# Kernel tuning notes

Measured on AMD Instinct MI355X. Metric: run time of the kernel, lower is better.

The kernel has to match this reference:

```python
import jax, jax.numpy as jnp
import numpy as np

VOCAB, ED, HW, HS, NC = 100000, 200, 100, 100, 10
B, S, W = 128, 40, 50


def setup_inputs() -> dict:
    key = jax.random.key(0)
    ks = jax.random.split(key, 24)
    def p(k, shape, s=0.05):
        return jax.random.normal(k, shape, dtype=jnp.float32) * s
    emb = p(ks[0], (VOCAB, ED)).at[VOCAB - 1].set(0.0)  # padding_idx = vocab-1
    d = dict(
        x=jax.random.randint(ks[23], (B, S, W), 0, VOCAB),
        emb=emb,
        # word bidirectional GRU (forward + backward cells), torch gate order r,z,n
        w_Wih_f=p(ks[1], (3 * HW, ED)), w_bih_f=p(ks[2], (3 * HW,)), w_bhh_f=p(ks[3], (3 * HW,)),
        w_Wih_b=p(ks[4], (3 * HW, ED)), w_bih_b=p(ks[5], (3 * HW,)), w_bhh_b=p(ks[6], (3 * HW,)),
        # word attention
        wa_W=p(ks[7], (2 * HW, 2 * HW)), wa_b=p(ks[8], (2 * HW,)), wa_ctx=p(ks[9], (2 * HW,)),
        # sentence bidirectional GRU (input = 2*HW)
        s_Wih_f=p(ks[10], (3 * HS, 2 * HW)), s_bih_f=p(ks[11], (3 * HS,)), s_bhh_f=p(ks[12], (3 * HS,)),
        s_Wih_b=p(ks[13], (3 * HS, 2 * HW)), s_bih_b=p(ks[14], (3 * HS,)), s_bhh_b=p(ks[15], (3 * HS,)),
        # sentence attention
        sa_W=p(ks[16], (2 * HS, 2 * HS)), sa_b=p(ks[17], (2 * HS,)), sa_ctx=p(ks[18], (2 * HS,)),
        # classifier
        fc_W=p(ks[19], (NC, 2 * HS)), fc_b=p(ks[20], (NC,)),
    )
    return d


def _gru0(x, Wih, bih, bhh, H):
    # GRU cell from zero hidden state: W_hh @ h0 == 0, only b_hh survives.
    g = x @ Wih.T + bih  # [..., 3H], gate order r, z, n
    r = jax.nn.sigmoid(g[..., :H] + bhh[:H])
    z = jax.nn.sigmoid(g[..., H:2 * H] + bhh[H:2 * H])
    n = jnp.tanh(g[..., 2 * H:] + r * bhh[2 * H:])
    return (1.0 - z) * n  # h' = (1-z)*n + z*0


def _bigru0(x, Wf, bf, bhf, Wb, bb, bhb, H):
    # one-timestep bidirectional GRU: fwd and bwd cells both see zero state
    return jnp.concatenate([_gru0(x, Wf, bf, bhf, H), _gru0(x, Wb, bb, bhb, H)], axis=-1)


def _attn(x, Wa, ba, ctx):
    # additive attention pooling over the second-to-last axis
    scores = jnp.einsum('...nd,d->...n', jnp.tanh(x @ Wa.T + ba), ctx)
    alpha = jax.nn.softmax(scores, axis=-1)
    return jnp.einsum('...n,...nd->...d', alpha, x)


def reference(x, emb, w_Wih_f, w_bih_f, w_bhh_f, w_Wih_b, w_bih_b, w_bhh_b,
              wa_W, wa_b, wa_ctx, s_Wih_f, s_bih_f, s_bhh_f, s_Wih_b, s_bih_b, s_bhh_b,
              sa_W, sa_b, sa_ctx, fc_W, fc_b):
    e = emb[x]                                                   # [B,S,W,ED]
    wenc = _bigru0(e, w_Wih_f, w_bih_f, w_bhh_f, w_Wih_b, w_bih_b, w_bhh_b, HW)  # [B,S,W,2HW]
    svec = _attn(wenc, wa_W, wa_b, wa_ctx)                       # [B,S,2HW]
    senc = _bigru0(svec, s_Wih_f, s_bih_f, s_bhh_f, s_Wih_b, s_bih_b, s_bhh_b, HS)  # [B,S,2HS]
    dvec = _attn(senc, sa_W, sa_b, sa_ctx)                       # [B,2HS]
    logits = dvec @ fc_W.T + fc_b                                # [B,NC]
    return jax.nn.log_softmax(logits, axis=1)
```

## Files before the change

### kernel.cpp

```cpp
#include <hip/hip_runtime.h>
#include <math.h>

#define NB    128
#define NS    40
#define NW    50
#define ED    200
#define NHW   100
#define FEAT  200
#define NC    10
#define VOCABM1 99999
#define KL2E  1.4426950408889634f

#define BB       20736ull
#define OFF_PGW  0ull
#define OFF_PAW  (14ull*BB)
#define OFF_PGS  (OFF_PAW + 5ull*BB)
#define OFF_PAS  (OFF_PGS + 14ull*BB)
#define OFF_SV   846336ull
#define OFF_DV   2894336ull
#define WS_NEED  4194304ull

#define SLOT   20736
#define HST    400
#define HBYTES 20000

typedef short bf16x8 __attribute__((ext_vector_type(8)));
typedef float f32x4  __attribute__((ext_vector_type(4)));
typedef unsigned u32x4 __attribute__((ext_vector_type(4)));

__device__ __forceinline__ unsigned short f2bf(float f) {
    unsigned int u = __float_as_uint(f);
    u += 0x7fffu + ((u >> 16) & 1u);
    return (unsigned short)(u >> 16);
}
__device__ __forceinline__ float bf2f(short s) {
    return __uint_as_float(((unsigned int)(unsigned short)s) << 16);
}
__device__ __forceinline__ float frcp(float x) { return __builtin_amdgcn_rcpf(x); }
#if __has_builtin(__builtin_amdgcn_exp2f)
__device__ __forceinline__ float fexp2(float x){ return __builtin_amdgcn_exp2f(x); }
#else
__device__ __forceinline__ float fexp2(float x){ return exp2f(x); }
#endif
__device__ __forceinline__ float fsig(float x) { return frcp(1.f + __expf(-x)); }
__device__ __forceinline__ float ftanh(float x){ return 1.f - 2.f*frcp(1.f + __expf(2.f*x)); }

__device__ __forceinline__ unsigned cvtpk(float lo, float hi) {
    unsigned r;
    asm("v_cvt_pk_bf16_f32 %0, %1, %2" : "=v"(r) : "v"(lo), "v"(hi));
    return r;
}

__device__ __forceinline__ void gld16(const void* g, void* l) {
    __builtin_amdgcn_global_load_lds(
        (const __attribute__((address_space(1))) void*)g,
        (__attribute__((address_space(3))) void*)l, 16, 0, 0);
}

__device__ __forceinline__ void stageBlob(char* __restrict__ dst,
                                          const char* __restrict__ src, int tid)
{
    #pragma unroll
    for (int u = 0; u < 5; ++u)
        gld16(src + (size_t)(u * 256 + tid) * 16, dst + (size_t)(u * 256 + tid) * 16);
    if (tid < 16)
        gld16(src + (size_t)(1280 + tid) * 16, dst + (size_t)(1280 + tid) * 16);
}

__device__ __forceinline__ bf16x8 pack8(float4 a, float4 b) {
    u32x4 t;
    t[0] = cvtpk(a.x, a.y); t[1] = cvtpk(a.z, a.w);
    t[2] = cvtpk(b.x, b.y); t[3] = cvtpk(b.z, b.w);
    return __builtin_bit_cast(bf16x8, t);
}

__global__ void pack_kernel(
    const float* __restrict__ wWf, const float* __restrict__ wbif, const float* __restrict__ wbhf,
    const float* __restrict__ wWb, const float* __restrict__ wbib, const float* __restrict__ wbhb,
    const float* __restrict__ waW, const float* __restrict__ wab, const float* __restrict__ wactx,
    const float* __restrict__ sWf, const float* __restrict__ sbif, const float* __restrict__ sbhf,
    const float* __restrict__ sWb, const float* __restrict__ sbib, const float* __restrict__ sbhb,
    const float* __restrict__ saW, const float* __restrict__ sab, const float* __restrict__ sactx,
    char* __restrict__ ws)
{
    const int b = blockIdx.x, tid = threadIdx.x;
    const bool word = b < 19;
    const int lb = word ? b : b - 19;
    char* blob;
    if (lb < 14) blob = ws + (word ? OFF_PGW : OFF_PGS) + (size_t)lb * BB;
    else         blob = ws + (word ? OFF_PAW : OFF_PAS) + (size_t)(lb - 14) * BB;

    for (int i = tid; i < (int)(BB / 4); i += 256) ((unsigned*)blob)[i] = 0u;
    __syncthreads();

    unsigned short* w16 = (unsigned short*)blob;
    if (lb < 14) {
        const int dir = lb / 7, c = lb % 7;
        const float* W   = word ? (dir ? wWb : wWf) : (dir ? sWb : sWf);
        const float* bih = word ? (dir ? wbib : wbif) : (dir ? sbib : sbif);
        const float* bhh = word ? (dir ? wbhb : wbhf) : (dir ? sbhb : sbhf);
        for (int e = tid; e < 48 * 200; e += 256) {
            const int row = e / 200, k = e - row * 200;
            const int gate = row >> 4, j = c * 16 + (row & 15);
            if (j < NHW) w16[row * 216 + k] = f2bf(W[(size_t)(gate * NHW + j) * ED + k]);
        }
        if (tid < 64) {
            const int sect = tid >> 4, j = c * 16 + (tid & 15);
            float v = 0.f;
            if (j < NHW) {
                if (sect == 0)      v = -KL2E * (bih[j] + bhh[j]);
                else if (sect == 1) v =  KL2E * (bih[NHW + j] + bhh[NHW + j]);
                else if (sect == 2) v = 2.f * KL2E * bih[2 * NHW + j];
                else                v = 2.f * KL2E * bhh[2 * NHW + j];
            }
            ((float*)(blob + (size_t)(tid >> 2) * 432 + 400))[tid & 3] = v;
        }
    } else {
        const int cb = lb - 14;
        const float* W  = word ? waW : saW;
        const float* ab = word ? wab : sab;
        const float* cx = word ? wactx : sactx;
        for (int e = tid; e < 48 * 200; e += 256) {
            const int row = e / 200, k = e - row * 200;
            const int d = cb * 48 + row;
            if (d < FEAT) w16[row * 216 + k] = f2bf(W[(size_t)d * FEAT + k]);
        }
        if (tid < 48) {
            const int d = cb * 48 + tid;
            float ab2 = 0.f, cxn = 0.f;
            if (d < FEAT) { ab2 = 2.f * KL2E * ab[d]; cxn = -2.f * cx[d]; }
            ((float*)(blob + (size_t)(tid >> 2) * 432 + 400))[tid & 3] = ab2;
            ((float*)(blob + (size_t)(12 + (tid >> 2)) * 432 + 400))[tid & 3] = cxn;
        }
    }
}

template<bool WORD>
__global__ __launch_bounds__(256, 4) void han_kernel(
    const int* __restrict__ xtok,
    const void* __restrict__ Ain,
    const char* __restrict__ gpk,
    const char* __restrict__ apk,
    const int nvalid,
    unsigned short* __restrict__ Out)
{
    __shared__ __align__(16) char smem[2 * SLOT + 2 * HBYTES];
    char* bufs = smem;
    char* Hsh  = smem + 2 * SLOT;

    const int tid  = threadIdx.x;
    const int lane = tid & 63, wv = tid >> 6;
    const int sent = wv >> 1, half = wv & 1;
    const int ln15 = lane & 15, q = lane >> 4;
    const long g   = (long)blockIdx.x * 2 + sent;
    char* Hme = Hsh + (size_t)sent * HBYTES;
    float* sc_sh = (float*)Hme;
    float* al_sh = (float*)(Hme + 256);
    float* part  = (float*)(Hme + 512);

    stageBlob(bufs, gpk, tid);

    bf16x8 af[2][7];
    if (WORD) {
        const float* emb = (const float*)Ain;
        #pragma unroll
        for (int Mt = 0; Mt < 2; ++Mt) {
            const int item = half * 32 + Mt * 16 + ln15;
            int tok = VOCABM1;
            if (item < nvalid) tok = xtok[g * nvalid + item];
            const float4* rp = (const float4*)(emb + (long)tok * ED);
            #pragma unroll
            for (int kc = 0; kc < 6; ++kc)
                af[Mt][kc] = pack8(rp[kc * 8 + q * 2], rp[kc * 8 + q * 2 + 1]);
            af[Mt][6] = (q == 0) ? pack8(rp[48], rp[49]) : (bf16x8)(short)0;
        }
    } else {
        const char* sv = (const char*)Ain;
        #pragma unroll
        for (int Mt = 0; Mt < 2; ++Mt) {
            const int item = half * 32 + Mt * 16 + ln15;
            const int ic = item < nvalid ? item : nvalid - 1;
            const char* rp = sv + (g * nvalid + ic) * 400;
            #pragma unroll
            for (int kc = 0; kc < 7; ++kc) {
                bf16x8 v = (bf16x8)(short)0;
                if (item < nvalid && (kc < 6 || q == 0))
                    v = *(const bf16x8*)(rp + kc * 64 + q * 16);
                af[Mt][kc] = v;
            }
        }
    }

    __syncthreads();

    bf16x8 hf[2][7];
    float sacc[2][4] = {{0.f}};

    for (int s = 0; s < 19; ++s) {
        {
            const int t = (s + 1 <= 18) ? (s + 1) : 18;
            const char* nb = (t < 14) ? gpk + (size_t)t * BB
                                      : apk + (size_t)(t - 14) * BB;
            stageBlob(bufs + (size_t)((s + 1) & 1) * SLOT, nb, tid);
        }
        char* cur = bufs + (size_t)(s & 1) * SLOT;

        if (s < 14) {
            f32x4 a0[2] = {}, a1[2] = {}, a2[2] = {};
            #pragma unroll
            for (int kc = 0; kc < 7; ++kc) {
                bf16x8 b0 = (bf16x8)(short)0, b1 = (bf16x8)(short)0, b2 = (bf16x8)(short)0;
                if (kc < 6 || q == 0) {
                    b0 = *(const bf16x8*)(cur + (size_t)(0  + ln15) * 432 + kc * 64 + q * 16);
                    b1 = *(const bf16x8*)(cur + (size_t)(16 + ln15) * 432 + kc * 64 + q * 16);
                    b2 = *(const bf16x8*)(cur + (size_t)(32 + ln15) * 432 + kc * 64 + q * 16);
                }
                #pragma unroll
                for (int Mt = 0; Mt < 2; ++Mt) {
                    a0[Mt] = __builtin_amdgcn_mfma_f32_16x16x32_bf16(b0, af[Mt][kc], a0[Mt], 0, 0, 0);
                    a1[Mt] = __builtin_amdgcn_mfma_f32_16x16x32_bf16(b1, af[Mt][kc], a1[Mt], 0, 0, 0);
                    a2[Mt] = __builtin_amdgcn_mfma_f32_16x16x32_bf16(b2, af[Mt][kc], a2[Mt], 0, 0, 0);
                }
            }
            const int dir = s / 7, cc = s - dir * 7;
            if (cc * 16 + q * 4 < NHW) {
                const f32x4 bR = *(const f32x4*)(cur + (size_t)(0  + q) * 432 + 400);
                const f32x4 bZ = *(const f32x4*)(cur + (size_t)(4  + q) * 432 + 400);
                const f32x4 bN = *(const f32x4*)(cur + (size_t)(8  + q) * 432 + 400);
                const f32x4 hN = *(const f32x4*)(cur + (size_t)(12 + q) * 432 + 400);
                const int ub = dir * NHW + cc * 16 + q * 4;
                #pragma unroll
                for (int Mt = 0; Mt < 2; ++Mt) {
                    const int item = half * 32 + Mt * 16 + ln15;
                    float h[4];
                    #pragma unroll
                    for (int rg = 0; rg < 4; ++rg) {
                        const float r  = frcp(1.f + fexp2(fmaf(a0[Mt][rg], -KL2E, bR[rg])));
                        const float zc = frcp(1.f + fexp2(fmaf(a1[Mt][rg],  KL2E, bZ[rg])));
                        const float t  = frcp(1.f + fexp2(fmaf(a2[Mt][rg], 2.f * KL2E,
                                                  fmaf(r, hN[rg], bN[rg]))));
                        h[rg] = zc * (1.f - 2.f * t);
                    }
                    if (item < nvalid) {
                        uint2 o; o.x = cvtpk(h[0], h[1]); o.y = cvtpk(h[2], h[3]);
                        *(uint2*)(Hme + (size_t)item * HST + ub * 2) = o;
                    }
                }
            }
        } else {
            if (s == 14) {
                #pragma unroll
                for (int Mt = 0; Mt < 2; ++Mt) {
                    const int item = half * 32 + Mt * 16 + ln15;
                    #pragma unroll
                    for (int kc = 0; kc < 7; ++kc) {
                        bf16x8 v = (bf16x8)(short)0;
                        if (item < nvalid && (kc < 6 || q == 0))
                            v = *(const bf16x8*)(Hme + (size_t)item * HST + kc * 64 + q * 16);
                        hf[Mt][kc] = v;
                    }
                }
            }
            f32x4 ac[2][3] = {};
            #pragma unroll
            for (int kc = 0; kc < 7; ++kc) {
                bf16x8 b0 = (bf16x8)(short)0, b1 = (bf16x8)(short)0, b2 = (bf16x8)(short)0;
                if (kc < 6 || q == 0) {
                    b0 = *(const bf16x8*)(cur + (size_t)(0  + ln15) * 432 + kc * 64 + q * 16);
                    b1 = *(const bf16x8*)(cur + (size_t)(16 + ln15) * 432 + kc * 64 + q * 16);
                    b2 = *(const bf16x8*)(cur + (size_t)(32 + ln15) * 432 + kc * 64 + q * 16);
                }
                #pragma unroll
                for (int Mt = 0; Mt < 2; ++Mt) {
                    ac[Mt][0] = __builtin_amdgcn_mfma_f32_16x16x32_bf16(hf[Mt][kc], b0, ac[Mt][0], 0, 0, 0);
                    ac[Mt][1] = __builtin_amdgcn_mfma_f32_16x16x32_bf16(hf[Mt][kc], b1, ac[Mt][1], 0, 0, 0);
                    ac[Mt][2] = __builtin_amdgcn_mfma_f32_16x16x32_bf16(hf[Mt][kc], b2, ac[Mt][2], 0, 0, 0);
                }
            }
            #pragma unroll
            for (int Nt = 0; Nt < 3; ++Nt) {
                const int bo = 4 * (Nt * 16 + ln15);
                const float ab2 = *(const float*)(cur + (size_t)(bo >> 4) * 432 + 400 + (bo & 15));
                const int co = 192 + bo;
                const float cxn = *(const float*)(cur + (size_t)(co >> 4) * 432 + 400 + (co & 15));
                #pragma unroll
                for (int Mt = 0; Mt < 2; ++Mt)
                    #pragma unroll
                    for (int rg = 0; rg < 4; ++rg) {
                        const float u = frcp(1.f + fexp2(fmaf(ac[Mt][Nt][rg], 2.f * KL2E, ab2)));
                        sacc[Mt][rg] = fmaf(u, cxn, sacc[Mt][rg]);
                    }
            }
        }
        __syncthreads();
    }

    #pragma unroll
    for (int Mt = 0; Mt < 2; ++Mt)
        #pragma unroll
        for (int rg = 0; rg < 4; ++rg) {
            float v = sacc[Mt][rg];
            v += __shfl_xor(v, 1); v += __shfl_xor(v, 2);
            v += __shfl_xor(v, 4); v += __shfl_xor(v, 8);
            sacc[Mt][rg] = v;
        }
    if (ln15 == 0) {
        #pragma unroll
        for (int Mt = 0; Mt < 2; ++Mt)
            #pragma unroll
            for (int rg = 0; rg < 4; ++rg)
                sc_sh[half * 32 + Mt * 16 + q * 4 + rg] = sacc[Mt][rg];
    }
    __syncthreads();

    {
        const float sv0 = (lane < nvalid) ? sc_sh[lane] : -1e30f;
        float m = sv0;
        m = fmaxf(m, __shfl_xor(m, 1));  m = fmaxf(m, __shfl_xor(m, 2));
        m = fmaxf(m, __shfl_xor(m, 4));  m = fmaxf(m, __shfl_xor(m, 8));
        m = fmaxf(m, __shfl_xor(m, 16)); m = fmaxf(m, __shfl_xor(m, 32));
        const float e = (lane < nvalid) ? fexp2((sv0 - m) * KL2E) : 0.f;
        float ss = e;
        ss += __shfl_xor(ss, 1);  ss += __shfl_xor(ss, 2);
        ss += __shfl_xor(ss, 4);  ss += __shfl_xor(ss, 8);
        ss += __shfl_xor(ss, 16); ss += __shfl_xor(ss, 32);
        if (half == 0) al_sh[lane] = e * frcp(ss);
    }
    __syncthreads();

    {
        const float aM0 = al_sh[half * 32 + ln15];
        const float aM1 = al_sh[half * 32 + 16 + ln15];
        #pragma unroll
        for (int kc = 0; kc < 7; ++kc) {
            float p[8];
            #pragma unroll
            for (int j = 0; j < 8; ++j)
                p[j] = aM0 * bf2f(hf[0][kc][j]) + aM1 * bf2f(hf[1][kc][j]);
            #pragma unroll
            for (int j = 0; j < 8; ++j) {
                p[j] += __shfl_xor(p[j], 1); p[j] += __shfl_xor(p[j], 2);
                p[j] += __shfl_xor(p[j], 4); p[j] += __shfl_xor(p[j], 8);
            }
            if (ln15 == 0) {
                float* dst = part + (size_t)half * 224 + kc * 32 + q * 8;
                f32x4 v0 = {p[0], p[1], p[2], p[3]};
                f32x4 v1 = {p[4], p[5], p[6], p[7]};
                *(f32x4*)dst = v0; *(f32x4*)(dst + 4) = v1;
            }
        }
    }
    __syncthreads();

    if (tid < 100) {
        const int sl = tid / 50, i = tid - sl * 50;
        const float* pg = (const float*)(Hsh + (size_t)sl * HBYTES + 512);
        const float* pa = pg;
        const float* pb = pg + 224;
        uint2 o;
        o.x = cvtpk(pa[i * 4 + 0] + pb[i * 4 + 0], pa[i * 4 + 1] + pb[i * 4 + 1]);
        o.y = cvtpk(pa[i * 4 + 2] + pb[i * 4 + 2], pa[i * 4 + 3] + pb[i * 4 + 3]);
        *(uint2*)(Out + ((long)blockIdx.x * 2 + sl) * 200 + i * 4) = o;
    }
}

__global__ void cls_kernel(const unsigned short* __restrict__ dvec,
                           const float* __restrict__ fcW, const float* __restrict__ fcb,
                           float* __restrict__ out)
{
    const int doc = blockIdx.x, lane = threadIdx.x;
    const int c = lane & 15, part = lane >> 4;
    const int cs = (c < NC) ? c : 0;
    float acc = (part == 0 && c < NC) ? fcb[c] : 0.f;
    for (int i = 0; i < 50; ++i) {
        const int k = part * 50 + i;
        const float a = bf2f((short)dvec[(size_t)doc * 200 + k]);
        acc += a * ((c < NC) ? fcW[(size_t)cs * 200 + k] : 0.f);
    }
    acc += __shfl_xor(acc, 16); acc += __shfl_xor(acc, 32);
    const float lg = (c < NC) ? acc : -1e30f;
    float m = lg;
    m = fmaxf(m, __shfl_xor(m, 1)); m = fmaxf(m, __shfl_xor(m, 2));
    m = fmaxf(m, __shfl_xor(m, 4)); m = fmaxf(m, __shfl_xor(m, 8));
    const float e = (c < NC) ? __expf(lg - m) : 0.f;
    float ss = e;
    ss += __shfl_xor(ss, 1); ss += __shfl_xor(ss, 2);
    ss += __shfl_xor(ss, 4); ss += __shfl_xor(ss, 8);
    const float lse = m + __logf(ss);
    if (lane < NC) out[(size_t)doc * NC + lane] = lg - lse;
}

template<int NWRD, int WT>
__device__ __forceinline__ void encode_block(
    float* __restrict__ e_sh, float* __restrict__ h_sh, float* __restrict__ sc_sh,
    const float* __restrict__ Wf, const float* __restrict__ bihf, const float* __restrict__ bhhf,
    const float* __restrict__ Wb, const float* __restrict__ bihb, const float* __restrict__ bhhb,
    const float* __restrict__ aW, const float* __restrict__ ab, const float* __restrict__ actx,
    int tid)
{
    constexpr int WG = NWRD / WT;
    for (int item = tid; item < FEAT * WG; item += 256) {
        const int unit = item % FEAT, wg = item / FEAT;
        const int dir = unit / NHW, j = unit - dir * NHW;
        const float* Wd  = dir ? Wb : Wf;
        const float* bih = dir ? bihb : bihf;
        const float* bhh = dir ? bhhb : bhhf;
        const float4* rowR = (const float4*)(Wd + (size_t)j * ED);
        const float4* rowZ = (const float4*)(Wd + (size_t)(NHW + j) * ED);
        const float4* rowN = (const float4*)(Wd + (size_t)(2 * NHW + j) * ED);
        float aR[WT], aZ[WT], aN[WT];
        #pragma unroll
        for (int t = 0; t < WT; ++t) { aR[t] = 0.f; aZ[t] = 0.f; aN[t] = 0.f; }
        const int w0 = wg * WT;
        #pragma unroll 1
        for (int k4 = 0; k4 < ED / 4; ++k4) {
            const float4 wr = rowR[k4], wz = rowZ[k4], wn = rowN[k4];
            #pragma unroll
            for (int t = 0; t < WT; ++t) {
                const float4 e = *(const float4*)(e_sh + (w0 + t) * ED + k4 * 4);
                aR[t] += wr.x*e.x + wr.y*e.y + wr.z*e.z + wr.w*e.w;
                aZ[t] += wz.x*e.x + wz.y*e.y + wz.z*e.z + wz.w*e.w;
                aN[t] += wn.x*e.x + wn.y*e.y + wn.z*e.z + wn.w*e.w;
            }
        }
        const float bR = bih[j] + bhh[j], bZ = bih[NHW+j] + bhh[NHW+j];
        const float bN = bih[2*NHW+j], hN = bhh[2*NHW+j];
        #pragma unroll
        for (int t = 0; t < WT; ++t) {
            const float r = fsig(aR[t] + bR), z = fsig(aZ[t] + bZ);
            const float n = ftanh(aN[t] + bN + r * hN);
            h_sh[(w0 + t) * FEAT + unit] = (1.f - z) * n;
        }
    }
    __syncthreads();
    for (int item = tid; item < FEAT * WG; item += 256) {
        const int d = item % FEAT, wg = item / FEAT;
        const float4* row = (const float4*)(aW + (size_t)d * FEAT);
        float acc[WT];
        #pragma unroll
        for (int t = 0; t < WT; ++t) acc[t] = 0.f;
        const int w0 = wg * WT;
        #pragma unroll 1
        for (int k4 = 0; k4 < FEAT / 4; ++k4) {
            const float4 wv = row[k4];
            #pragma unroll
            for (int t = 0; t < WT; ++t) {
                const float4 h = *(const float4*)(h_sh + (w0 + t) * FEAT + k4 * 4);
                acc[t] += wv.x*h.x + wv.y*h.y + wv.z*h.z + wv.w*h.w;
            }
        }
        const float bb = ab[d], cc = actx[d];
        #pragma unroll
        for (int t = 0; t < WT; ++t)
            e_sh[d * NWRD + (w0 + t)] = ftanh(acc[t] + bb) * cc;
    }
    __syncthreads();
    if (tid < NWRD) {
        float s = 0.f;
        for (int d = 0; d < FEAT; ++d) s += e_sh[d * NWRD + tid];
        sc_sh[tid] = s;
    }
    __syncthreads();
    if (tid == 0) {
        float m = -1e30f;
        for (int w = 0; w < NWRD; ++w) m = fmaxf(m, sc_sh[w]);
        float s = 0.f;
        for (int w = 0; w < NWRD; ++w) { const float ev = __expf(sc_sh[w] - m); sc_sh[w] = ev; s += ev; }
        const float inv = 1.f / s;
        for (int w = 0; w < NWRD; ++w) sc_sh[w] *= inv;
    }
    __syncthreads();
}

__global__ __launch_bounds__(256) void word_kernel_f32(
    const int* __restrict__ x, const float* __restrict__ emb,
    const float* __restrict__ Wf, const float* __restrict__ bihf, const float* __restrict__ bhhf,
    const float* __restrict__ Wb, const float* __restrict__ bihb, const float* __restrict__ bhhb,
    const float* __restrict__ waW, const float* __restrict__ wab, const float* __restrict__ wactx,
    float* __restrict__ svec)
{
    __shared__ __align__(16) float e_sh[NW * ED];
    __shared__ __align__(16) float h_sh[NW * FEAT];
    __shared__ float sc_sh[NW];
    const int sent = blockIdx.x, tid = threadIdx.x;
    const int* xr = x + (size_t)sent * NW;
    for (int i = tid * 4; i < NW * ED; i += 256 * 4) {
        const int w = i / ED, k = i - w * ED;
        *(float4*)(e_sh + i) = *(const float4*)(emb + (size_t)xr[w] * ED + k);
    }
    __syncthreads();
    encode_block<NW, 25>(e_sh, h_sh, sc_sh, Wf, bihf, bhhf, Wb, bihb, bhhb, waW, wab, wactx, tid);
    if (tid < FEAT) {
        float a = 0.f;
        #pragma unroll 1
        for (int w = 0; w < NW; ++w) a += sc_sh[w] * h_sh[w * FEAT + tid];
        svec[(size_t)sent * FEAT + tid] = a;
    }
}

__global__ __launch_bounds__(256) void sent_kernel_f32(
    const float* __restrict__ svec,
    const float* __restrict__ Wf, const float* __restrict__ bihf, const float* __restrict__ bhhf,
    const float* __restrict__ Wb, const float* __restrict__ bihb, const float* __restrict__ bhhb,
    const float* __restrict__ saW, const float* __restrict__ sab, const float* __restrict__ sactx,
    const float* __restrict__ fcW, const float* __restrict__ fcb,
    float* __restrict__ out)
{
    __shared__ __align__(16) float e_sh[NS * ED];
    __shared__ __align__(16) float h_sh[NS * FEAT];
    __shared__ float sc_sh[NS];
    __shared__ float dvec_sh[FEAT];
    __shared__ float logit_sh[NC];
    __shared__ float lse_sh;
    const int b = blockIdx.x, tid = threadIdx.x;
    const float* src = svec + (size_t)b * NS * FEAT;
    for (int i = tid * 4; i < NS * FEAT; i += 256 * 4)
        *(float4*)(e_sh + i) = *(const float4*)(src + i);
    __syncthreads();
    encode_block<NS, 20>(e_sh, h_sh, sc_sh, Wf, bihf, bhhf, Wb, bihb, bhhb, saW, sab, sactx, tid);
    if (tid < FEAT) {
        float a = 0.f;
        #pragma unroll 1
        for (int s = 0; s < NS; ++s) a += sc_sh[s] * h_sh[s * FEAT + tid];
        dvec_sh[tid] = a;
    }
    __syncthreads();
    if (tid < NC) {
        float a = fcb[tid];
        const float* row = fcW + (size_t)tid * FEAT;
        for (int k = 0; k < FEAT; ++k) a += row[k] * dvec_sh[k];
        logit_sh[tid] = a;
    }
    __syncthreads();
    if (tid == 0) {
        float m = -1e30f;
        for (int c = 0; c < NC; ++c) m = fmaxf(m, logit_sh[c]);
        float s = 0.f;
        for (int c = 0; c < NC; ++c) s += __expf(logit_sh[c] - m);
        lse_sh = m + logf(s);
    }
    __syncthreads();
    if (tid < NC) out[(size_t)b * NC + tid] = logit_sh[tid] - lse_sh;
}

extern "C" void kernel_launch(void* const* d_in, const int* in_sizes, int n_in,
                              void* d_out, int out_size, void* d_ws, size_t ws_size,
                              hipStream_t stream)
{
    const int*   x     = (const int*)d_in[0];
    const float* emb   = (const float*)d_in[1];
    const float* wWf   = (const float*)d_in[2];
    const float* wbif  = (const float*)d_in[3];
    const float* wbhf  = (const float*)d_in[4];
    const float* wWb   = (const float*)d_in[5];
    const float* wbib  = (const float*)d_in[6];
    const float* wbhb  = (const float*)d_in[7];
    const float* waW   = (const float*)d_in[8];
    const float* wab   = (const float*)d_in[9];
    const float* wactx = (const float*)d_in[10];
    const float* sWf   = (const float*)d_in[11];
    const float* sbif  = (const float*)d_in[12];
    const float* sbhf  = (const float*)d_in[13];
    const float* sWb   = (const float*)d_in[14];
    const float* sbib  = (const float*)d_in[15];
    const float* sbhb  = (const float*)d_in[16];
    const float* saW   = (const float*)d_in[17];
    const float* sab   = (const float*)d_in[18];
    const float* sactx = (const float*)d_in[19];
    const float* fcW   = (const float*)d_in[20];
    const float* fcb   = (const float*)d_in[21];
    float* out = (float*)d_out;

    if (ws_size < WS_NEED) {
        float* svec = (float*)d_ws;
        word_kernel_f32<<<NB * NS, 256, 0, stream>>>(
            x, emb, wWf, wbif, wbhf, wWb, wbib, wbhb, waW, wab, wactx, svec);
        sent_kernel_f32<<<NB, 256, 0, stream>>>(
            svec, sWf, sbif, sbhf, sWb, sbib, sbhb, saW, sab, sactx, fcW, fcb, out);
        return;
    }

    char* ws = (char*)d_ws;
    unsigned short* svec = (unsigned short*)(ws + OFF_SV);
    unsigned short* dvec = (unsigned short*)(ws + OFF_DV);

    pack_kernel<<<38, 256, 0, stream>>>(
        wWf, wbif, wbhf, wWb, wbib, wbhb, waW, wab, wactx,
        sWf, sbif, sbhf, sWb, sbib, sbhb, saW, sab, sactx, ws);

    han_kernel<true><<<NB * NS / 2, 256, 0, stream>>>(
        x, emb, ws + OFF_PGW, ws + OFF_PAW, NW, svec);

    han_kernel<false><<<NB / 2, 256, 0, stream>>>(
        nullptr, svec, ws + OFF_PGS, ws + OFF_PAS, NS, dvec);

    cls_kernel<<<NB, 64, 0, stream>>>(dvec, fcW, fcb, out);
}
```

Measured before the change: 400.5 us.

## Read packed weights directly from global in MFMA fragment order, drop LDS staging

The weight packing is rewritten so each 16-row by 32-k block is stored in the exact per-lane bf16x8 fragment order the MFMA needs. The main kernel then reads B fragments straight from global/L2 instead of double-buffering blobs through LDS with global_load_lds, which removes the per-step barriers and frees most of the shared memory. The sentence-level launch now uses one sentence group per 128-thread block to spread work over more blocks. In exchange, every wave re-reads the weights from cache each step, so it depends on L2/L1 hit rates rather than LDS bandwidth.

After: 802.9 us. +100.5%, slower.

```diff
diff --git a/kernel.cpp b/kernel.cpp
--- a/kernel.cpp
+++ b/kernel.cpp
@@ -11,16 +11,11 @@
 #define VOCABM1 99999
 #define KL2E  1.4426950408889634f
 
-#define BB       20736ull
-#define OFF_PGW  0ull
-#define OFF_PAW  (14ull*BB)
-#define OFF_PGS  (OFF_PAW + 5ull*BB)
-#define OFF_PAS  (OFF_PGS + 14ull*BB)
+#define BBn      22016ull
 #define OFF_SV   846336ull
 #define OFF_DV   2894336ull
 #define WS_NEED  4194304ull
 
-#define SLOT   20736
 #define HST    400
 #define HBYTES 20000
 
@@ -35,6 +30,9 @@
 }
 __device__ __forceinline__ float bf2f(short s) {
     return __uint_as_float(((unsigned int)(unsigned short)s) << 16);
+}
+__device__ __forceinline__ unsigned pk2(float a, float b) {
+    return (unsigned)f2bf(a) | ((unsigned)f2bf(b) << 16);
 }
 __device__ __forceinline__ float frcp(float x) { return __builtin_amdgcn_rcpf(x); }
 #if __has_builtin(__builtin_amdgcn_exp2f)
@@ -50,23 +48,6 @@
     asm("v_cvt_pk_bf16_f32 %0, %1, %2" : "=v"(r) : "v"(lo), "v"(hi));
     return r;
 }
-
-__device__ __forceinline__ void gld16(const void* g, void* l) {
-    __builtin_amdgcn_global_load_lds(
-        (const __attribute__((address_space(1))) void*)g,
-        (__attribute__((address_space(3))) void*)l, 16, 0, 0);
-}
-
-__device__ __forceinline__ void stageBlob(char* __restrict__ dst,
-                                          const char* __restrict__ src, int tid)
-{
-    #pragma unroll
-    for (int u = 0; u < 5; ++u)
-        gld16(src + (size_t)(u * 256 + tid) * 16, dst + (size_t)(u * 256 + tid) * 16);
-    if (tid < 16)
-        gld16(src + (size_t)(1280 + tid) * 16, dst + (size_t)(1280 + tid) * 16);
-}
-
 __device__ __forceinline__ bf16x8 pack8(float4 a, float4 b) {
     u32x4 t;
     t[0] = cvtpk(a.x, a.y); t[1] = cvtpk(a.z, a.w);
@@ -86,26 +67,28 @@
     const int b = blockIdx.x, tid = threadIdx.x;
     const bool word = b < 19;
     const int lb = word ? b : b - 19;
-    char* blob;
-    if (lb < 14) blob = ws + (word ? OFF_PGW : OFF_PGS) + (size_t)lb * BB;
-    else         blob = ws + (word ? OFF_PAW : OFF_PAS) + (size_t)(lb - 14) * BB;
-
-    for (int i = tid; i < (int)(BB / 4); i += 256) ((unsigned*)blob)[i] = 0u;
-    __syncthreads();
-
-    unsigned short* w16 = (unsigned short*)blob;
+    char* blob = ws + (size_t)b * BBn;
+
     if (lb < 14) {
         const int dir = lb / 7, c = lb % 7;
         const float* W   = word ? (dir ? wWb : wWf) : (dir ? sWb : sWf);
         const float* bih = word ? (dir ? wbib : wbif) : (dir ? sbib : sbif);
         const float* bhh = word ? (dir ? wbhb : wbhf) : (dir ? sbhb : sbhf);
-        for (int e = tid; e < 48 * 200; e += 256) {
-            const int row = e / 200, k = e - row * 200;
-            const int gate = row >> 4, j = c * 16 + (row & 15);
-            if (j < NHW) w16[row * 216 + k] = f2bf(W[(size_t)(gate * NHW + j) * ED + k]);
+        for (int e = tid; e < 21 * 64; e += 256) {
+            const int f = e >> 6, l = e & 63;
+            const int g = f % 3, kc = f / 3;
+            const int j = c * 16 + (l & 15);
+            const int k0 = kc * 32 + (l >> 4) * 8;
+            u32x4 out = {0u, 0u, 0u, 0u};
+            if (j < NHW && k0 < 200) {
+                const float* src = W + (size_t)(g * NHW + j) * ED + k0;
+                out[0] = pk2(src[0], src[1]); out[1] = pk2(src[2], src[3]);
+                out[2] = pk2(src[4], src[5]); out[3] = pk2(src[6], src[7]);
+            }
+            *(u32x4*)(blob + ((size_t)f << 10) + (size_t)l * 16) = out;
         }
         if (tid < 64) {
-            const int sect = tid >> 4, j = c * 16 + (tid & 15);
+            const int sect = tid >> 4, idx = tid & 15, j = c * 16 + idx;
             float v = 0.f;
             if (j < NHW) {
                 if (sect == 0)      v = -KL2E * (bih[j] + bhh[j]);
@@ -113,52 +96,55 @@
                 else if (sect == 2) v = 2.f * KL2E * bih[2 * NHW + j];
                 else                v = 2.f * KL2E * bhh[2 * NHW + j];
             }
-            ((float*)(blob + (size_t)(tid >> 2) * 432 + 400))[tid & 3] = v;
+            *(float*)(blob + 21504 + sect * 64 + idx * 4) = v;
         }
     } else {
         const int cb = lb - 14;
         const float* W  = word ? waW : saW;
         const float* ab = word ? wab : sab;
         const float* cx = word ? wactx : sactx;
-        for (int e = tid; e < 48 * 200; e += 256) {
-            const int row = e / 200, k = e - row * 200;
-            const int d = cb * 48 + row;
-            if (d < FEAT) w16[row * 216 + k] = f2bf(W[(size_t)d * FEAT + k]);
+        for (int e = tid; e < 21 * 64; e += 256) {
+            const int f = e >> 6, l = e & 63;
+            const int g = f % 3, kc = f / 3;
+            const int d = cb * 48 + g * 16 + (l & 15);
+            const int k0 = kc * 32 + (l >> 4) * 8;
+            u32x4 out = {0u, 0u, 0u, 0u};
+            if (d < FEAT && k0 < 200) {
+                const float* src = W + (size_t)d * FEAT + k0;
+                out[0] = pk2(src[0], src[1]); out[1] = pk2(src[2], src[3]);
+                out[2] = pk2(src[4], src[5]); out[3] = pk2(src[6], src[7]);
+            }
+            *(u32x4*)(blob + ((size_t)f << 10) + (size_t)l * 16) = out;
         }
         if (tid < 48) {
             const int d = cb * 48 + tid;
             float ab2 = 0.f, cxn = 0.f;
             if (d < FEAT) { ab2 = 2.f * KL2E * ab[d]; cxn = -2.f * cx[d]; }
-            ((float*)(blob + (size_t)(tid >> 2) * 432 + 400))[tid & 3] = ab2;
-            ((float*)(blob + (size_t)(12 + (tid >> 2)) * 432 + 400))[tid & 3] = cxn;
-        }
-    }
-}
-
-template<bool WORD>
-__global__ __launch_bounds__(256, 4) void han_kernel(
+            *(float*)(blob + 21504 + tid * 4) = ab2;
+            *(float*)(blob + 21696 + tid * 4) = cxn;
+        }
+    }
+}
+
+template<bool WORD, int NG>
+__global__ __launch_bounds__(NG * 128, 3) void han_kernel(
     const int* __restrict__ xtok,
     const void* __restrict__ Ain,
-    const char* __restrict__ gpk,
-    const char* __restrict__ apk,
+    const char* __restrict__ pk,
     const int nvalid,
     unsigned short* __restrict__ Out)
 {
-    __shared__ __align__(16) char smem[2 * SLOT + 2 * HBYTES];
-    char* bufs = smem;
-    char* Hsh  = smem + 2 * SLOT;
+    __shared__ __align__(16) char Hsh[NG * HBYTES];
 
     const int tid  = threadIdx.x;
     const int lane = tid & 63, wv = tid >> 6;
     const int sent = wv >> 1, half = wv & 1;
     const int ln15 = lane & 15, q = lane >> 4;
-    const long g   = (long)blockIdx.x * 2 + sent;
+    const long g   = (long)blockIdx.x * NG + sent;
     char* Hme = Hsh + (size_t)sent * HBYTES;
     float* sc_sh = (float*)Hme;
     float* al_sh = (float*)(Hme + 256);
     float* part  = (float*)(Hme + 512);
-
-    stageBlob(bufs, gpk, tid);
 
     bf16x8 af[2][7];
     if (WORD) {
@@ -191,30 +177,21 @@
         }
     }
 
-    __syncthreads();
-
     bf16x8 hf[2][7];
     float sacc[2][4] = {{0.f}};
 
+    #pragma unroll 1
     for (int s = 0; s < 19; ++s) {
-        {
-            const int t = (s + 1 <= 18) ? (s + 1) : 18;
-            const char* nb = (t < 14) ? gpk + (size_t)t * BB
-                                      : apk + (size_t)(t - 14) * BB;
-            stageBlob(bufs + (size_t)((s + 1) & 1) * SLOT, nb, tid);
-        }
-        char* cur = bufs + (size_t)(s & 1) * SLOT;
+        const char* blob = pk + (size_t)s * BBn;
+        const char* fb   = blob + (size_t)lane * 16;
 
         if (s < 14) {
             f32x4 a0[2] = {}, a1[2] = {}, a2[2] = {};
             #pragma unroll
             for (int kc = 0; kc < 7; ++kc) {
-                bf16x8 b0 = (bf16x8)(short)0, b1 = (bf16x8)(short)0, b2 = (bf16x8)(short)0;
-                if (kc < 6 || q == 0) {
-                    b0 = *(const bf16x8*)(cur + (size_t)(0  + ln15) * 432 + kc * 64 + q * 16);
-                    b1 = *(const bf16x8*)(cur + (size_t)(16 + ln15) * 432 + kc * 64 + q * 16);
-                    b2 = *(const bf16x8*)(cur + (size_t)(32 + ln15) * 432 + kc * 64 + q * 16);
-                }
+                const bf16x8 b0 = *(const bf16x8*)(fb + ((kc * 3 + 0) << 10));
+                const bf16x8 b1 = *(const bf16x8*)(fb + ((kc * 3 + 1) << 10));
+                const bf16x8 b2 = *(const bf16x8*)(fb + ((kc * 3 + 2) << 10));
                 #pragma unroll
                 for (int Mt = 0; Mt < 2; ++Mt) {
                     a0[Mt] = __builtin_amdgcn_mfma_f32_16x16x32_bf16(b0, af[Mt][kc], a0[Mt], 0, 0, 0);
@@ -224,10 +201,10 @@
             }
             const int dir = s / 7, cc = s - dir * 7;
             if (cc * 16 + q * 4 < NHW) {
-                const f32x4 bR = *(const f32x4*)(cur + (size_t)(0  + q) * 432 + 400);
-                const f32x4 bZ = *(const f32x4*)(cur + (size_t)(4  + q) * 432 + 400);
-                const f32x4 bN = *(const f32x4*)(cur + (size_t)(8  + q) * 432 + 400);
-                const f32x4 hN = *(const f32x4*)(cur + (size_t)(12 + q) * 432 + 400);
+                const f32x4 bR = *(const f32x4*)(blob + 21504 +   0 + q * 16);
+                const f32x4 bZ = *(const f32x4*)(blob + 21504 +  64 + q * 16);
+                const f32x4 bN = *(const f32x4*)(blob + 21504 + 128 + q * 16);
+                const f32x4 hN = *(const f32x4*)(blob + 21504 + 192 + q * 16);
                 const int ub = dir * NHW + cc * 16 + q * 4;
                 #pragma unroll
                 for (int Mt = 0; Mt < 2; ++Mt) {
@@ -264,12 +241,9 @@
             f32x4 ac[2][3] = {};
             #pragma unroll
             for (int kc = 0; kc < 7; ++kc) {
-                bf16x8 b0 = (bf16x8)(short)0, b1 = (bf16x8)(short)0, b2 = (bf16x8)(short)0;
-                if (kc < 6 || q == 0) {
-                    b0 = *(const bf16x8*)(cur + (size_t)(0  + ln15) * 432 + kc * 64 + q * 16);
-                    b1 = *(const bf16x8*)(cur + (size_t)(16 + ln15) * 432 + kc * 64 + q * 16);
-                    b2 = *(const bf16x8*)(cur + (size_t)(32 + ln15) * 432 + kc * 64 + q * 16);
-                }
+                const bf16x8 b0 = *(const bf16x8*)(fb + ((kc * 3 + 0) << 10));
+                const bf16x8 b1 = *(const bf16x8*)(fb + ((kc * 3 + 1) << 10));
+                const bf16x8 b2 = *(const bf16x8*)(fb + ((kc * 3 + 2) << 10));
                 #pragma unroll
                 for (int Mt = 0; Mt < 2; ++Mt) {
                     ac[Mt][0] = __builtin_amdgcn_mfma_f32_16x16x32_bf16(hf[Mt][kc], b0, ac[Mt][0], 0, 0, 0);
@@ -279,10 +253,8 @@
             }
             #pragma unroll
             for (int Nt = 0; Nt < 3; ++Nt) {
-                const int bo = 4 * (Nt * 16 + ln15);
-                const float ab2 = *(const float*)(cur + (size_t)(bo >> 4) * 432 + 400 + (bo & 15));
-                const int co = 192 + bo;
-                const float cxn = *(const float*)(cur + (size_t)(co >> 4) * 432 + 400 + (co & 15));
+                const float ab2 = *(const float*)(blob + 21504 + (Nt * 16 + ln15) * 4);
+                const float cxn = *(const float*)(blob + 21696 + (Nt * 16 + ln15) * 4);
                 #pragma unroll
                 for (int Mt = 0; Mt < 2; ++Mt)
                     #pragma unroll
@@ -292,7 +264,6 @@
                     }
             }
         }
-        __syncthreads();
     }
 
     #pragma unroll
@@ -304,6 +275,9 @@
             v += __shfl_xor(v, 4); v += __shfl_xor(v, 8);
             sacc[Mt][rg] = v;
         }
+
+    __syncthreads();
+
     if (ln15 == 0) {
         #pragma unroll
         for (int Mt = 0; Mt < 2; ++Mt)
@@ -352,7 +326,7 @@
     }
     __syncthreads();
 
-    if (tid < 100) {
+    if (tid < NG * 50) {
         const int sl = tid / 50, i = tid - sl * 50;
         const float* pg = (const float*)(Hsh + (size_t)sl * HBYTES + 512);
         const float* pa = pg;
@@ -360,7 +334,7 @@
         uint2 o;
         o.x = cvtpk(pa[i * 4 + 0] + pb[i * 4 + 0], pa[i * 4 + 1] + pb[i * 4 + 1]);
         o.y = cvtpk(pa[i * 4 + 2] + pb[i * 4 + 2], pa[i * 4 + 3] + pb[i * 4 + 3]);
-        *(uint2*)(Out + ((long)blockIdx.x * 2 + sl) * 200 + i * 4) = o;
+        *(uint2*)(Out + ((long)blockIdx.x * NG + sl) * 200 + i * 4) = o;
     }
 }
 
@@ -588,11 +562,11 @@
         wWf, wbif, wbhf, wWb, wbib, wbhb, waW, wab, wactx,
         sWf, sbif, sbhf, sWb, sbib, sbhb, saW, sab, sactx, ws);
 
-    han_kernel<true><<<NB * NS / 2, 256, 0, stream>>>(
-        x, emb, ws + OFF_PGW, ws + OFF_PAW, NW, svec);
-
-    han_kernel<false><<<NB / 2, 256, 0, stream>>>(
-        nullptr, svec, ws + OFF_PGS, ws + OFF_PAS, NS, dvec);
+    han_kernel<true, 2><<<NB * NS / 2, 256, 0, stream>>>(
+        x, emb, ws, NW, svec);
+
+    han_kernel<false, 1><<<NB, 128, 0, stream>>>(
+        nullptr, svec, ws + 19ull * BBn, NS, dvec);
 
     cls_kernel<<<NB, 64, 0, stream>>>(dvec, fcW, fcb, out);
 }
```
